# Performance work log

Measured on AMD Instinct MI355X. Metric: run time of the kernel, lower is better.

## Reference

```python
import jax, jax.numpy as jnp
import numpy as np

STATE_DIM, SKILL_DIM = 256, 64
HID = 1024
LAT = 128
B = 4096
TEMP = 1.0


def _init_linear(key, fan_in, fan_out):
    # torch nn.Linear default init: U(-1/sqrt(fan_in), 1/sqrt(fan_in))
    kw, kb = jax.random.split(key)
    bound = 1.0 / np.sqrt(fan_in)
    W = jax.random.uniform(kw, (fan_in, fan_out), jnp.float32, -bound, bound)
    b = jax.random.uniform(kb, (fan_out,), jnp.float32, -bound, bound)
    return W, b


def setup_inputs() -> dict:
    key = jax.random.key(0)
    ks = jax.random.split(key, 8)
    x = jax.random.normal(ks[0], (B, STATE_DIM), jnp.float32)
    y = jax.random.normal(ks[1], (B, SKILL_DIM), jnp.float32)
    sW1, sb1 = _init_linear(ks[2], STATE_DIM, HID)
    sW2, sb2 = _init_linear(ks[3], HID, HID)
    sW3, sb3 = _init_linear(ks[4], HID, LAT)
    kW1, kb1 = _init_linear(ks[5], SKILL_DIM, HID)
    kW2, kb2 = _init_linear(ks[6], HID, HID)
    kW3, kb3 = _init_linear(ks[7], HID, LAT)
    return {
        "x": x, "y": y,
        "sW1": sW1, "sb1": sb1, "sW2": sW2, "sb2": sb2, "sW3": sW3, "sb3": sb3,
        "kW1": kW1, "kb1": kb1, "kW2": kW2, "kb2": kb2, "kW3": kW3, "kb3": kb3,
    }


def _mlp(x, W1, b1, W2, b2, W3, b3):
    h = jax.nn.relu(x @ W1 + b1)
    h = jax.nn.relu(h @ W2 + b2)
    return h @ W3 + b3


def _l2norm(v, eps=1e-12):
    # matches F.normalize(dim=-1): v / max(||v||, eps)
    n = jnp.sqrt(jnp.sum(v * v, axis=-1, keepdims=True))
    return v / jnp.maximum(n, eps)


def reference(x, y, sW1, sb1, sW2, sb2, sW3, sb3, kW1, kb1, kW2, kb2, kW3, kb3):
    zx = _l2norm(_mlp(x, sW1, sb1, sW2, sb2, sW3, sb3))  # [B, LAT]
    zy = _l2norm(_mlp(y, kW1, kb1, kW2, kb2, kW3, kb3))  # [B, LAT]
    # sum(x[:,None,:]*y[None,:,:], -1) == zx @ zy.T (same math, no BxBxD blowup)
    scores = jnp.einsum('id,jd->ij', zx, zy) / TEMP       # [B, B]
    # InfoNCE lower bound: log(B) - CE(scores, arange(B)), reduction='none'
    logp = jax.nn.log_softmax(scores, axis=-1)
    nll = jnp.diagonal(logp)                               # = -CE per row
    mi = jnp.log(jnp.float32(scores.shape[0])) + nll       # [B]
    return scores, mi
```

## Files before the change

kernel.cpp:

```cpp
#include <hip/hip_runtime.h>
#include <hip/hip_bf16.h>
#include <math.h>

typedef __bf16 v8bf __attribute__((ext_vector_type(8)));
typedef float  v4f  __attribute__((ext_vector_type(4)));

#define GPTR(p) ((const __attribute__((address_space(1))) void*)(p))
#define LPTR(p) ((__attribute__((address_space(3))) void*)(p))

struct PrepArgs {
    const float* x; const float* y;
    __hip_bfloat16* xb; __hip_bfloat16* yb;
    int nx4, ntot4;
    const float* wsrc[6];
    __hip_bfloat16* wdst[6];
    int K[6], N[6];
};

__global__ __launch_bounds__(256)
void prep_k(PrepArgs a) {
    const int tid = threadIdx.x, bx = blockIdx.x, z = blockIdx.z;
    if (z == 0) {
        int i = bx * 256 + tid;
        if (i >= a.ntot4) return;
        const float* src; __hip_bfloat16* dst; int j;
        if (i < a.nx4) { src = a.x; dst = a.xb; j = i; }
        else           { src = a.y; dst = a.yb; j = i - a.nx4; }
        float4 v = ((const float4*)src)[j];
        __hip_bfloat16 h[4] = {__float2bfloat16(v.x), __float2bfloat16(v.y),
                               __float2bfloat16(v.z), __float2bfloat16(v.w)};
        ((short4*)dst)[j] = *(short4*)h;
        return;
    }
    int w = z - 1;
    int K = a.K[w], N = a.N[w];
    int tn = N >> 5;
    int tt = (K >> 5) * tn;
    if (bx >= tt) return;
    int kt = (bx / tn) * 32, nt = (bx % tn) * 32;
    __shared__ float t[32][33];
    int tx = tid & 31, ty = tid >> 5;
    const float* W = a.wsrc[w];
    __hip_bfloat16* Wt = a.wdst[w];
#pragma unroll
    for (int i = 0; i < 4; ++i)
        t[ty + i * 8][tx] = W[(size_t)(kt + ty + i * 8) * N + nt + tx];
    __syncthreads();
#pragma unroll
    for (int i = 0; i < 4; ++i)
        Wt[(size_t)(nt + ty + i * 8) * K + kt + tx] =
            __float2bfloat16(t[tx][ty + i * 8]);
}

__device__ __forceinline__ void gemm_mainloop(
    const __hip_bfloat16* __restrict__ A, const __hip_bfloat16* __restrict__ Bt,
    int lda, int ldb, int kbeg, int kend, int bm, int bn,
    int wid, int lane, int wr, int wc,
    __hip_bfloat16* As, __hip_bfloat16* Bs, v4f acc[4][4]) {
    const int crow = lane >> 3;
    const int ccol = (lane & 7) * 8;
    for (int k0 = kbeg; k0 < kend; k0 += 64) {
#pragma unroll
        for (int i = 0; i < 4; ++i) {
            int c = wid * 4 + i;
            __builtin_amdgcn_global_load_lds(
                GPTR(A + (size_t)(bm + c * 8 + crow) * lda + k0 + ccol),
                LPTR(As + c * 512), 16, 0, 0);
            __builtin_amdgcn_global_load_lds(
                GPTR(Bt + (size_t)(bn + c * 8 + crow) * ldb + k0 + ccol),
                LPTR(Bs + c * 512), 16, 0, 0);
        }
        __syncthreads();
#pragma unroll
        for (int kk = 0; kk < 64; kk += 32) {
            v8bf a[4], b[4];
#pragma unroll
            for (int i = 0; i < 4; ++i) {
                a[i] = *(const v8bf*)&As[(wr * 64 + i * 16 + (lane & 15)) * 64 + kk + (lane >> 4) * 8];
                b[i] = *(const v8bf*)&Bs[(wc * 64 + i * 16 + (lane & 15)) * 64 + kk + (lane >> 4) * 8];
            }
#pragma unroll
            for (int i = 0; i < 4; ++i)
#pragma unroll
                for (int j = 0; j < 4; ++j)
                    acc[i][j] = __builtin_amdgcn_mfma_f32_16x16x32_bf16(
                        a[i], b[j], acc[i][j], 0, 0, 0);
        }
        __syncthreads();
    }
}

struct MlpArgs {
    const __hip_bfloat16* A[2];
    const __hip_bfloat16* B[2];
    const float* bias[2];
    __hip_bfloat16* C[2];
    int K[2];
};

__global__ __launch_bounds__(256)
void gemm_mlp_k(MlpArgs args) {
    __shared__ __align__(16) __hip_bfloat16 As[128 * 64], Bs[128 * 64];
    const int z = blockIdx.z;
    const int tid = threadIdx.x, wid = tid >> 6, lane = tid & 63;
    const int wr = wid >> 1, wc = wid & 1;
    const int bm = blockIdx.x * 128, bn = blockIdx.y * 128;
    const int K = args.K[z];
    v4f acc[4][4] = {};
    gemm_mainloop(args.A[z], args.B[z], K, K, 0, K, bm, bn, wid, lane, wr, wc,
                  As, Bs, acc);
    const float* bias = args.bias[z];
    __hip_bfloat16* C = args.C[z];
#pragma unroll
    for (int i = 0; i < 4; ++i) {
        int rowb = bm + wr * 64 + i * 16 + (lane >> 4) * 4;
#pragma unroll
        for (int j = 0; j < 4; ++j) {
            int col = bn + wc * 64 + j * 16 + (lane & 15);
            float bv = bias[col];
#pragma unroll
            for (int r = 0; r < 4; ++r) {
                float v = fmaxf(acc[i][j][r] + bv, 0.f);
                C[(size_t)(rowb + r) * 1024 + col] = __float2bfloat16(v);
            }
        }
    }
}

__global__ __launch_bounds__(256)
void gemm_l3norm_k(const __hip_bfloat16* __restrict__ As_g0,
                   const __hip_bfloat16* __restrict__ As_g1,
                   const __hip_bfloat16* __restrict__ Bt0,
                   const __hip_bfloat16* __restrict__ Bt1,
                   const float* __restrict__ sb3, const float* __restrict__ kb3,
                   __hip_bfloat16* __restrict__ zxb,
                   __hip_bfloat16* __restrict__ zyb) {
    __shared__ __align__(16) __hip_bfloat16 As[32 * 64];
    __shared__ __align__(16) __hip_bfloat16 Bs[128 * 64];
    __shared__ float red[4][32];
    const int z = blockIdx.y;
    const __hip_bfloat16* A  = z ? As_g1 : As_g0;
    const __hip_bfloat16* Bt = z ? Bt1 : Bt0;
    const float* bias = z ? kb3 : sb3;
    __hip_bfloat16* zout = z ? zyb : zxb;

    const int tid = threadIdx.x, wid = tid >> 6, lane = tid & 63;
    const int bm = blockIdx.x * 32;
    const int crow = lane >> 3, ccol = (lane & 7) * 8;

    v4f acc[2][2] = {};
    for (int k0 = 0; k0 < 1024; k0 += 64) {
        __builtin_amdgcn_global_load_lds(
            GPTR(A + (size_t)(bm + wid * 8 + crow) * 1024 + k0 + ccol),
            LPTR(As + wid * 512), 16, 0, 0);
#pragma unroll
        for (int i = 0; i < 4; ++i) {
            int c = wid * 4 + i;
            __builtin_amdgcn_global_load_lds(
                GPTR(Bt + (size_t)(c * 8 + crow) * 1024 + k0 + ccol),
                LPTR(Bs + c * 512), 16, 0, 0);
        }
        __syncthreads();
#pragma unroll
        for (int kk = 0; kk < 64; kk += 32) {
            v8bf a[2], b[2];
#pragma unroll
            for (int i = 0; i < 2; ++i)
                a[i] = *(const v8bf*)&As[(i * 16 + (lane & 15)) * 64 + kk + (lane >> 4) * 8];
#pragma unroll
            for (int j = 0; j < 2; ++j)
                b[j] = *(const v8bf*)&Bs[(wid * 32 + j * 16 + (lane & 15)) * 64 + kk + (lane >> 4) * 8];
#pragma unroll
            for (int i = 0; i < 2; ++i)
#pragma unroll
                for (int j = 0; j < 2; ++j)
                    acc[i][j] = __builtin_amdgcn_mfma_f32_16x16x32_bf16(
                        a[i], b[j], acc[i][j], 0, 0, 0);
        }
        __syncthreads();
    }

    float val[2][2][4];
    float ssq[2][4];
#pragma unroll
    for (int i = 0; i < 2; ++i)
#pragma unroll
        for (int r = 0; r < 4; ++r) ssq[i][r] = 0.f;
#pragma unroll
    for (int i = 0; i < 2; ++i)
#pragma unroll
        for (int j = 0; j < 2; ++j) {
            int col = wid * 32 + j * 16 + (lane & 15);
            float bv = bias[col];
#pragma unroll
            for (int r = 0; r < 4; ++r) {
                float v = acc[i][j][r] + bv;
                val[i][j][r] = v;
                ssq[i][r] += v * v;
            }
        }
#pragma unroll
    for (int i = 0; i < 2; ++i)
#pragma unroll
        for (int r = 0; r < 4; ++r) {
#pragma unroll
            for (int m = 1; m < 16; m <<= 1)
                ssq[i][r] += __shfl_xor(ssq[i][r], m, 64);
            if ((lane & 15) == 0)
                red[wid][i * 16 + (lane >> 4) * 4 + r] = ssq[i][r];
        }
    __syncthreads();
#pragma unroll
    for (int i = 0; i < 2; ++i)
#pragma unroll
        for (int r = 0; r < 4; ++r) {
            int row = i * 16 + (lane >> 4) * 4 + r;
            float ss = red[0][row] + red[1][row] + red[2][row] + red[3][row];
            float inv = 1.0f / fmaxf(sqrtf(ss), 1e-12f);
#pragma unroll
            for (int j = 0; j < 2; ++j) {
                int col = wid * 32 + j * 16 + (lane & 15);
                zout[(size_t)(bm + row) * 128 + col] =
                    __float2bfloat16(val[i][j][r] * inv);
            }
        }
}

__global__ __launch_bounds__(256)
void gemm_scores_k(const __hip_bfloat16* __restrict__ zxb,
                   const __hip_bfloat16* __restrict__ zyb,
                   float* __restrict__ out, float* __restrict__ esum) {
    __shared__ __align__(16) __hip_bfloat16 As[128 * 64], Bs[128 * 64];
    __shared__ float rowsum[2][128];
    const int tid = threadIdx.x, wid = tid >> 6, lane = tid & 63;
    const int wr = wid >> 1, wc = wid & 1;
    const int bm = blockIdx.x * 128, bn = blockIdx.y * 128;
    v4f acc[4][4] = {};
    gemm_mainloop(zxb, zyb, 128, 128, 0, 128, bm, bn, wid, lane, wr, wc,
                  As, Bs, acc);
#pragma unroll
    for (int i = 0; i < 4; ++i) {
        int rowb = bm + wr * 64 + i * 16 + (lane >> 4) * 4;
#pragma unroll
        for (int r = 0; r < 4; ++r) {
            float s = 0.f;
#pragma unroll
            for (int j = 0; j < 4; ++j) {
                int col = bn + wc * 64 + j * 16 + (lane & 15);
                float v = acc[i][j][r];
                __builtin_nontemporal_store(v, &out[(size_t)(rowb + r) * 4096 + col]);
                s += __expf(v - 1.0f);
            }
#pragma unroll
            for (int m = 1; m < 16; m <<= 1) s += __shfl_xor(s, m, 64);
            if ((lane & 15) == 0)
                rowsum[wc][wr * 64 + i * 16 + (lane >> 4) * 4 + r] = s;
        }
    }
    __syncthreads();
    if (tid < 128)
        esum[(size_t)(bm + tid) * 32 + blockIdx.y] =
            rowsum[0][tid] + rowsum[1][tid];
}

__global__ __launch_bounds__(256)
void mi_k(const float* __restrict__ esum, const float* __restrict__ scores,
          float* __restrict__ mi) {
    int row = blockIdx.x * 256 + threadIdx.x;
    const float4* p = (const float4*)&esum[(size_t)row * 32];
    float s = 0.f;
#pragma unroll
    for (int i = 0; i < 8; ++i) { float4 v = p[i]; s += v.x + v.y + v.z + v.w; }
    float diag = scores[(size_t)row * 4096 + row];
    mi[row] = 8.317766166719343f + diag - 1.0f - logf(s);
}

extern "C" void kernel_launch(void* const* d_in, const int* in_sizes, int n_in,
                              void* d_out, int out_size, void* d_ws, size_t ws_size,
                              hipStream_t stream) {
    const float* x   = (const float*)d_in[0];
    const float* y   = (const float*)d_in[1];
    const float* sW1 = (const float*)d_in[2];
    const float* sb1 = (const float*)d_in[3];
    const float* sW2 = (const float*)d_in[4];
    const float* sb2 = (const float*)d_in[5];
    const float* sW3 = (const float*)d_in[6];
    const float* sb3 = (const float*)d_in[7];
    const float* kW1 = (const float*)d_in[8];
    const float* kb1 = (const float*)d_in[9];
    const float* kW2 = (const float*)d_in[10];
    const float* kb2 = (const float*)d_in[11];
    const float* kW3 = (const float*)d_in[12];
    const float* kb3 = (const float*)d_in[13];

    float* out = (float*)d_out;
    float* mi  = out + (size_t)4096 * 4096;

    char* ws = (char*)d_ws;
    auto alloc = [&](size_t bytes) {
        char* p = ws;
        ws += (bytes + 255) & ~(size_t)255;
        return p;
    };
    __hip_bfloat16* xb   = (__hip_bfloat16*)alloc((size_t)4096 * 256 * 2);
    __hip_bfloat16* yb   = (__hip_bfloat16*)alloc((size_t)4096 * 64 * 2);
    __hip_bfloat16* sW1t = (__hip_bfloat16*)alloc((size_t)1024 * 256 * 2);
    __hip_bfloat16* sW2t = (__hip_bfloat16*)alloc((size_t)1024 * 1024 * 2);
    __hip_bfloat16* sW3t = (__hip_bfloat16*)alloc((size_t)128 * 1024 * 2);
    __hip_bfloat16* kW1t = (__hip_bfloat16*)alloc((size_t)1024 * 64 * 2);
    __hip_bfloat16* kW2t = (__hip_bfloat16*)alloc((size_t)1024 * 1024 * 2);
    __hip_bfloat16* kW3t = (__hip_bfloat16*)alloc((size_t)128 * 1024 * 2);
    __hip_bfloat16* h1s  = (__hip_bfloat16*)alloc((size_t)4096 * 1024 * 2);
    __hip_bfloat16* h1k  = (__hip_bfloat16*)alloc((size_t)4096 * 1024 * 2);
    __hip_bfloat16* h2s  = (__hip_bfloat16*)alloc((size_t)4096 * 1024 * 2);
    __hip_bfloat16* h2k  = (__hip_bfloat16*)alloc((size_t)4096 * 1024 * 2);
    float*          es   = (float*)alloc((size_t)4096 * 32 * 4);
    __hip_bfloat16* zxb  = (__hip_bfloat16*)alloc((size_t)4096 * 128 * 2);
    __hip_bfloat16* zyb  = (__hip_bfloat16*)alloc((size_t)4096 * 128 * 2);

    PrepArgs pa;
    pa.x = x; pa.y = y; pa.xb = xb; pa.yb = yb;
    pa.nx4 = 4096 * 256 / 4;
    pa.ntot4 = pa.nx4 + 4096 * 64 / 4;
    pa.wsrc[0] = sW1; pa.wdst[0] = sW1t; pa.K[0] = 256;  pa.N[0] = 1024;
    pa.wsrc[1] = sW2; pa.wdst[1] = sW2t; pa.K[1] = 1024; pa.N[1] = 1024;
    pa.wsrc[2] = sW3; pa.wdst[2] = sW3t; pa.K[2] = 1024; pa.N[2] = 128;
    pa.wsrc[3] = kW1; pa.wdst[3] = kW1t; pa.K[3] = 64;   pa.N[3] = 1024;
    pa.wsrc[4] = kW2; pa.wdst[4] = kW2t; pa.K[4] = 1024; pa.N[4] = 1024;
    pa.wsrc[5] = kW3; pa.wdst[5] = kW3t; pa.K[5] = 1024; pa.N[5] = 128;
    prep_k<<<dim3(1280, 1, 7), 256, 0, stream>>>(pa);

    MlpArgs l1;
    l1.A[0] = xb;  l1.B[0] = sW1t; l1.bias[0] = sb1; l1.C[0] = h1s; l1.K[0] = 256;
    l1.A[1] = yb;  l1.B[1] = kW1t; l1.bias[1] = kb1; l1.C[1] = h1k; l1.K[1] = 64;
    gemm_mlp_k<<<dim3(32, 8, 2), 256, 0, stream>>>(l1);

    MlpArgs l2;
    l2.A[0] = h1s; l2.B[0] = sW2t; l2.bias[0] = sb2; l2.C[0] = h2s; l2.K[0] = 1024;
    l2.A[1] = h1k; l2.B[1] = kW2t; l2.bias[1] = kb2; l2.C[1] = h2k; l2.K[1] = 1024;
    gemm_mlp_k<<<dim3(32, 8, 2), 256, 0, stream>>>(l2);

    gemm_l3norm_k<<<dim3(128, 2), 256, 0, stream>>>(
        h2s, h2k, sW3t, kW3t, sb3, kb3, zxb, zyb);

    gemm_scores_k<<<dim3(32, 32), 256, 0, stream>>>(zxb, zyb, out, es);

    mi_k<<<16, 256, 0, stream>>>(es, out, mi);
}
```

Baseline: 90.57 us.

## Double-buffer LDS tiles in MLP GEMMs and remap blocks for XCD locality

The MLP layer GEMMs and the layer-3 norm GEMM now keep two LDS buffers. Global-to-LDS loads for the next K tile are issued before computing the current one, with explicit vmcnt waits and barriers in place of full syncthreads. The grids are also flattened to 1D and block IDs remapped with a bid&7 stride so that blocks sharing A/B tiles land on the same XCD for L2 reuse. This doubles LDS use per block and may reduce occupancy, and the hand-picked vmcnt counts must match the number of loads issued per stage.

```diff
diff --git a/kernel.cpp b/kernel.cpp
--- a/kernel.cpp
+++ b/kernel.cpp
@@ -7,6 +7,15 @@
 
 #define GPTR(p) ((const __attribute__((address_space(1))) void*)(p))
 #define LPTR(p) ((__attribute__((address_space(3))) void*)(p))
+
+template <int N> __device__ __forceinline__ void waitvm() {
+    if constexpr (N == 0) asm volatile("s_waitcnt vmcnt(0)" ::: "memory");
+    else if constexpr (N == 5) asm volatile("s_waitcnt vmcnt(5)" ::: "memory");
+    else asm volatile("s_waitcnt vmcnt(8)" ::: "memory");
+}
+#define WAITLGKM() asm volatile("s_waitcnt lgkmcnt(0)" ::: "memory")
+#define BAR() __builtin_amdgcn_s_barrier()
+#define SCHEDBAR() __builtin_amdgcn_sched_barrier(0)
 
 struct PrepArgs {
     const float* x; const float* y;
@@ -52,41 +61,39 @@
             __float2bfloat16(t[tx][ty + i * 8]);
 }
 
-__device__ __forceinline__ void gemm_mainloop(
+__device__ __forceinline__ void stage128(
     const __hip_bfloat16* __restrict__ A, const __hip_bfloat16* __restrict__ Bt,
-    int lda, int ldb, int kbeg, int kend, int bm, int bn,
-    int wid, int lane, int wr, int wc,
-    __hip_bfloat16* As, __hip_bfloat16* Bs, v4f acc[4][4]) {
-    const int crow = lane >> 3;
-    const int ccol = (lane & 7) * 8;
-    for (int k0 = kbeg; k0 < kend; k0 += 64) {
+    int lda, int ldb, int bm, int bn, int k0, int wid, int crow, int ccol,
+    __hip_bfloat16* As, __hip_bfloat16* Bs) {
+#pragma unroll
+    for (int i = 0; i < 4; ++i) {
+        int c = wid * 4 + i;
+        __builtin_amdgcn_global_load_lds(
+            GPTR(A + (size_t)(bm + c * 8 + crow) * lda + k0 + ccol),
+            LPTR(As + c * 512), 16, 0, 0);
+        __builtin_amdgcn_global_load_lds(
+            GPTR(Bt + (size_t)(bn + c * 8 + crow) * ldb + k0 + ccol),
+            LPTR(Bs + c * 512), 16, 0, 0);
+    }
+}
+
+__device__ __forceinline__ void compute128(
+    const __hip_bfloat16* As, const __hip_bfloat16* Bs,
+    int lane, int wr, int wc, v4f acc[4][4]) {
+#pragma unroll
+    for (int kk = 0; kk < 64; kk += 32) {
+        v8bf a[4], b[4];
 #pragma unroll
         for (int i = 0; i < 4; ++i) {
-            int c = wid * 4 + i;
-            __builtin_amdgcn_global_load_lds(
-                GPTR(A + (size_t)(bm + c * 8 + crow) * lda + k0 + ccol),
-                LPTR(As + c * 512), 16, 0, 0);
-            __builtin_amdgcn_global_load_lds(
-                GPTR(Bt + (size_t)(bn + c * 8 + crow) * ldb + k0 + ccol),
-                LPTR(Bs + c * 512), 16, 0, 0);
-        }
-        __syncthreads();
-#pragma unroll
-        for (int kk = 0; kk < 64; kk += 32) {
-            v8bf a[4], b[4];
-#pragma unroll
-            for (int i = 0; i < 4; ++i) {
-                a[i] = *(const v8bf*)&As[(wr * 64 + i * 16 + (lane & 15)) * 64 + kk + (lane >> 4) * 8];
-                b[i] = *(const v8bf*)&Bs[(wc * 64 + i * 16 + (lane & 15)) * 64 + kk + (lane >> 4) * 8];
-            }
-#pragma unroll
-            for (int i = 0; i < 4; ++i)
-#pragma unroll
-                for (int j = 0; j < 4; ++j)
-                    acc[i][j] = __builtin_amdgcn_mfma_f32_16x16x32_bf16(
-                        a[i], b[j], acc[i][j], 0, 0, 0);
-        }
-        __syncthreads();
+            a[i] = *(const v8bf*)&As[(wr * 64 + i * 16 + (lane & 15)) * 64 + kk + (lane >> 4) * 8];
+            b[i] = *(const v8bf*)&Bs[(wc * 64 + i * 16 + (lane & 15)) * 64 + kk + (lane >> 4) * 8];
+        }
+#pragma unroll
+        for (int i = 0; i < 4; ++i)
+#pragma unroll
+            for (int j = 0; j < 4; ++j)
+                acc[i][j] = __builtin_amdgcn_mfma_f32_16x16x32_bf16(
+                    a[i], b[j], acc[i][j], 0, 0, 0);
     }
 }
 
@@ -100,15 +107,36 @@
 
 __global__ __launch_bounds__(256)
 void gemm_mlp_k(MlpArgs args) {
-    __shared__ __align__(16) __hip_bfloat16 As[128 * 64], Bs[128 * 64];
-    const int z = blockIdx.z;
+    __shared__ __align__(16) __hip_bfloat16 As[2][128 * 64], Bs[2][128 * 64];
+    const int bid = blockIdx.x;
+    const int wg  = (bid & 7) * 64 + (bid >> 3);
+    const int z   = wg >> 8;
+    const int rem = wg & 255;
+    const int bm  = (rem >> 3) * 128;
+    const int bn  = (rem & 7) * 128;
+
     const int tid = threadIdx.x, wid = tid >> 6, lane = tid & 63;
     const int wr = wid >> 1, wc = wid & 1;
-    const int bm = blockIdx.x * 128, bn = blockIdx.y * 128;
+    const int crow = lane >> 3, ccol = (lane & 7) * 8;
+    const __hip_bfloat16* A  = args.A[z];
+    const __hip_bfloat16* Bt = args.B[z];
     const int K = args.K[z];
+    const int nt = K >> 6;
+
     v4f acc[4][4] = {};
-    gemm_mainloop(args.A[z], args.B[z], K, K, 0, K, bm, bn, wid, lane, wr, wc,
-                  As, Bs, acc);
+    stage128(A, Bt, K, K, bm, bn, 0, wid, crow, ccol, As[0], Bs[0]);
+    int cur = 0;
+    for (int t = 0; t < nt - 1; ++t) {
+        stage128(A, Bt, K, K, bm, bn, (t + 1) * 64, wid, crow, ccol,
+                 As[cur ^ 1], Bs[cur ^ 1]);
+        waitvm<8>(); BAR(); SCHEDBAR();
+        compute128(As[cur], Bs[cur], lane, wr, wc, acc);
+        WAITLGKM(); BAR();
+        cur ^= 1;
+    }
+    waitvm<0>(); BAR(); SCHEDBAR();
+    compute128(As[cur], Bs[cur], lane, wr, wc, acc);
+
     const float* bias = args.bias[z];
     __hip_bfloat16* C = args.C[z];
 #pragma unroll
@@ -135,41 +163,44 @@
                    const float* __restrict__ sb3, const float* __restrict__ kb3,
                    __hip_bfloat16* __restrict__ zxb,
                    __hip_bfloat16* __restrict__ zyb) {
-    __shared__ __align__(16) __hip_bfloat16 As[32 * 64];
-    __shared__ __align__(16) __hip_bfloat16 Bs[128 * 64];
+    __shared__ __align__(16) __hip_bfloat16 As[2][32 * 64];
+    __shared__ __align__(16) __hip_bfloat16 Bs[2][128 * 64];
     __shared__ float red[4][32];
-    const int z = blockIdx.y;
+    const int bid = blockIdx.x;
+    const int wg  = (bid & 7) * 32 + (bid >> 3);
+    const int z   = wg >> 7;
+    const int bm  = (wg & 127) * 32;
+
     const __hip_bfloat16* A  = z ? As_g1 : As_g0;
     const __hip_bfloat16* Bt = z ? Bt1 : Bt0;
     const float* bias = z ? kb3 : sb3;
     __hip_bfloat16* zout = z ? zyb : zxb;
 
     const int tid = threadIdx.x, wid = tid >> 6, lane = tid & 63;
-    const int bm = blockIdx.x * 32;
     const int crow = lane >> 3, ccol = (lane & 7) * 8;
 
-    v4f acc[2][2] = {};
-    for (int k0 = 0; k0 < 1024; k0 += 64) {
+    auto stage = [&](int buf, int k0) {
         __builtin_amdgcn_global_load_lds(
             GPTR(A + (size_t)(bm + wid * 8 + crow) * 1024 + k0 + ccol),
-            LPTR(As + wid * 512), 16, 0, 0);
+            LPTR(&As[buf][wid * 512]), 16, 0, 0);
 #pragma unroll
         for (int i = 0; i < 4; ++i) {
             int c = wid * 4 + i;
             __builtin_amdgcn_global_load_lds(
                 GPTR(Bt + (size_t)(c * 8 + crow) * 1024 + k0 + ccol),
-                LPTR(Bs + c * 512), 16, 0, 0);
-        }
-        __syncthreads();
+                LPTR(&Bs[buf][c * 512]), 16, 0, 0);
+        }
+    };
+    auto compute = [&](int buf, v4f acc[2][2]) {
 #pragma unroll
         for (int kk = 0; kk < 64; kk += 32) {
             v8bf a[2], b[2];
 #pragma unroll
             for (int i = 0; i < 2; ++i)
-                a[i] = *(const v8bf*)&As[(i * 16 + (lane & 15)) * 64 + kk + (lane >> 4) * 8];
+                a[i] = *(const v8bf*)&As[buf][(i * 16 + (lane & 15)) * 64 + kk + (lane >> 4) * 8];
 #pragma unroll
             for (int j = 0; j < 2; ++j)
-                b[j] = *(const v8bf*)&Bs[(wid * 32 + j * 16 + (lane & 15)) * 64 + kk + (lane >> 4) * 8];
+                b[j] = *(const v8bf*)&Bs[buf][(wid * 32 + j * 16 + (lane & 15)) * 64 + kk + (lane >> 4) * 8];
 #pragma unroll
             for (int i = 0; i < 2; ++i)
 #pragma unroll
@@ -177,8 +208,20 @@
                     acc[i][j] = __builtin_amdgcn_mfma_f32_16x16x32_bf16(
                         a[i], b[j], acc[i][j], 0, 0, 0);
         }
-        __syncthreads();
-    }
+    };
+
+    v4f acc[2][2] = {};
+    stage(0, 0);
+    int cur = 0;
+    for (int t = 0; t < 15; ++t) {
+        stage(cur ^ 1, (t + 1) * 64);
+        waitvm<5>(); BAR(); SCHEDBAR();
+        compute(cur, acc);
+        WAITLGKM(); BAR();
+        cur ^= 1;
+    }
+    waitvm<0>(); BAR(); SCHEDBAR();
+    compute(cur, acc);
 
     float val[2][2][4];
     float ssq[2][4];
@@ -235,9 +278,15 @@
     const int tid = threadIdx.x, wid = tid >> 6, lane = tid & 63;
     const int wr = wid >> 1, wc = wid & 1;
     const int bm = blockIdx.x * 128, bn = blockIdx.y * 128;
+    const int crow = lane >> 3, ccol = (lane & 7) * 8;
     v4f acc[4][4] = {};
-    gemm_mainloop(zxb, zyb, 128, 128, 0, 128, bm, bn, wid, lane, wr, wc,
-                  As, Bs, acc);
+#pragma unroll
+    for (int t = 0; t < 2; ++t) {
+        stage128(zxb, zyb, 128, 128, bm, bn, t * 64, wid, crow, ccol, As, Bs);
+        __syncthreads();
+        compute128(As, Bs, lane, wr, wc, acc);
+        __syncthreads();
+    }
 #pragma unroll
     for (int i = 0; i < 4; ++i) {
         int rowb = bm + wr * 64 + i * 16 + (lane >> 4) * 4;
@@ -333,14 +382,14 @@
     MlpArgs l1;
     l1.A[0] = xb;  l1.B[0] = sW1t; l1.bias[0] = sb1; l1.C[0] = h1s; l1.K[0] = 256;
     l1.A[1] = yb;  l1.B[1] = kW1t; l1.bias[1] = kb1; l1.C[1] = h1k; l1.K[1] = 64;
-    gemm_mlp_k<<<dim3(32, 8, 2), 256, 0, stream>>>(l1);
+    gemm_mlp_k<<<512, 256, 0, stream>>>(l1);
 
     MlpArgs l2;
     l2.A[0] = h1s; l2.B[0] = sW2t; l2.bias[0] = sb2; l2.C[0] = h2s; l2.K[0] = 1024;
     l2.A[1] = h1k; l2.B[1] = kW2t; l2.bias[1] = kb2; l2.C[1] = h2k; l2.K[1] = 1024;
-    gemm_mlp_k<<<dim3(32, 8, 2), 256, 0, stream>>>(l2);
-
-    gemm_l3norm_k<<<dim3(128, 2), 256, 0, stream>>>(
+    gemm_mlp_k<<<512, 256, 0, stream>>>(l2);
+
+    gemm_l3norm_k<<<256, 256, 0, stream>>>(
         h2s, h2k, sW3t, kW3t, sb3, kb3, zxb, zyb);
 
     gemm_scores_k<<<dim3(32, 32), 256, 0, stream>>>(zxb, zyb, out, es);
```

Result: no change. 90.40 us (-0.2%).
